# Performance work log

Hardware: AMD Instinct MI355X
Metric: run time of the kernel (lower is better)

The kernel has to match this reference:

```python
import jax, jax.numpy as jnp
import numpy as np

NUM_GRAPHS = 32

def leaky(x):
    return jax.nn.leaky_relu(x, 0.1)

def setup_inputs() -> dict:
    key = jax.random.key(0)
    ks = jax.random.split(key, 32)
    N, E = 8000, 32000
    x = jax.random.normal(ks[0], (N, 4), dtype=jnp.float32)
    edge_index = jax.random.randint(ks[1], (2, E), 0, N, dtype=jnp.int32)
    batch_index = jnp.sort(jax.random.randint(ks[2], (N,), 0, NUM_GRAPHS, dtype=jnp.int32))
    def lin(k, i, o, s=0.1):
        k1, k2 = jax.random.split(k)
        return jax.random.normal(k1, (i, o), dtype=jnp.float32) * s, jax.random.normal(k2, (o,), dtype=jnp.float32) * s
    p = {}
    # edge networks: Linear(3,64)+LeakyReLU+Linear(64, in*out)+LeakyReLU
    p['en1_w1'], p['en1_b1'] = lin(ks[3], 3, 64)
    p['en1_w2'], p['en1_b2'] = lin(ks[4], 64, 4 * 8)
    p['en2_w1'], p['en2_b1'] = lin(ks[5], 3, 64)
    p['en2_w2'], p['en2_b2'] = lin(ks[6], 64, 8 * 64)
    p['en3_w1'], p['en3_b1'] = lin(ks[7], 3, 64)
    p['en3_w2'], p['en3_b2'] = lin(ks[8], 64, 64 * 128)
    # NNConv root weights + biases
    p['root1'], p['cb1'] = lin(ks[9], 4, 8)
    p['root2'], p['cb2'] = lin(ks[10], 8, 64)
    p['root3'], p['cb3'] = lin(ks[11], 64, 128)
    # readout MLP
    p['fc1_w'], p['fc1_b'] = lin(ks[12], 128, 128)
    p['fc2_w'], p['fc2_b'] = lin(ks[13], 128, 64)
    p['fc3_w'], p['fc3_b'] = lin(ks[14], 64, 1)
    return dict(x=x, edge_index=edge_index, batch_index=batch_index, **p)

def nnconv(h, edge_index, edge_attr, w1, b1, w2, b2, root, cbias, in_ch, out_ch):
    # per-edge weight matrix from edge attributes
    e = leaky(edge_attr @ w1 + b1)              # [E,64]
    W = leaky(e @ w2 + b2).reshape(-1, in_ch, out_ch)  # [E,in,out]
    msg = jnp.einsum('ei,eio->eo', h[edge_index[0]], W)  # gather + per-edge matmul
    agg = jax.ops.segment_sum(msg, edge_index[1], num_segments=h.shape[0])  # scatter-add
    return agg + h @ root + cbias

def reference(x, edge_index, batch_index, en1_w1, en1_b1, en1_w2, en1_b2, en2_w1, en2_b1, en2_w2, en2_b2, en3_w1, en3_b1, en3_w2, en3_b2, root1, cb1, root2, cb2, root3, cb3, fc1_w, fc1_b, fc2_w, fc2_b, fc3_w, fc3_b):
    edge_attr = (x[edge_index[1]] - x[edge_index[0]])[:, 1:]  # [E,3] relative position
    h = leaky(nnconv(x, edge_index, edge_attr, en1_w1, en1_b1, en1_w2, en1_b2, root1, cb1, 4, 8))
    h = leaky(nnconv(h, edge_index, edge_attr, en2_w1, en2_b1, en2_w2, en2_b2, root2, cb2, 8, 64))
    h = leaky(nnconv(h, edge_index, edge_attr, en3_w1, en3_b1, en3_w2, en3_b2, root3, cb3, 64, 128))
    g = jax.ops.segment_sum(h, batch_index, num_segments=NUM_GRAPHS)  # sum-pool per graph
    g = leaky(g @ fc1_w + fc1_b)
    g = leaky(g @ fc2_w + fc2_b)
    return g @ fc3_w + fc3_b  # [G,1] total energies
```

## Files before the change

kernel.cpp:

```cpp
#include <hip/hip_runtime.h>
#include <hip/hip_bf16.h>

typedef __attribute__((ext_vector_type(8))) short short8;
typedef __attribute__((ext_vector_type(4))) float floatx4;
typedef __attribute__((ext_vector_type(2))) float float2v;

__device__ __forceinline__ float leaky(float v){ return v > 0.f ? v : 0.1f*v; }
__device__ __forceinline__ void atomAdd(float* p, float v){ unsafeAtomicAdd(p, v); }
__device__ __forceinline__ short f2bf(float f){
  __hip_bfloat16 h = __float2bfloat16(f);
  return *reinterpret_cast<short*>(&h);
}

__global__ void efeat_conv1(const float* __restrict__ x, const int* __restrict__ ei,
                            const float* __restrict__ w1a, const float* __restrict__ b1a,
                            const float* __restrict__ w1b, const float* __restrict__ b1b,
                            const float* __restrict__ w1c, const float* __restrict__ b1c,
                            const float* __restrict__ c1w2, const float* __restrict__ c1b2,
                            short* __restrict__ ef2b, short* __restrict__ ef3b,
                            float* __restrict__ agg1, int E, int Epad){
  __shared__ float sm[4][64];
  int tid = threadIdx.x;
  int id = blockIdx.x*256 + tid;
  int e = id >> 6, j = id & 63;
  float v1 = 0.f;
  if (e < Epad){
    if (e >= E){ ef2b[id] = 0; ef3b[id] = 0; }
    else {
      int s = ei[e], d = ei[E+e];
      float a0 = x[d*4+1] - x[s*4+1];
      float a1 = x[d*4+2] - x[s*4+2];
      float a2 = x[d*4+3] - x[s*4+3];
      v1 = leaky(a0*w1a[j] + a1*w1a[64+j] + a2*w1a[128+j] + b1a[j]);
      ef2b[id] = f2bf(leaky(a0*w1b[j] + a1*w1b[64+j] + a2*w1b[128+j] + b1b[j]));
      ef3b[id] = f2bf(leaky(a0*w1c[j] + a1*w1c[64+j] + a2*w1c[128+j] + b1c[j]));
    }
  }
  sm[tid >> 6][j] = v1;
  __syncthreads();
  if (tid < 32){
    int le = tid >> 3, o = tid & 7;
    int ge = blockIdx.x*4 + le;
    if (ge < E){
      int s = ei[ge], d = ei[E+ge];
      float z[4];
      #pragma unroll
      for (int i=0;i<4;i++) z[i] = c1b2[i*8+o];
      for (int k=0;k<64;k++){
        float a = sm[le][k];
        #pragma unroll
        for (int i=0;i<4;i++) z[i] += a*c1w2[k*32 + i*8 + o];
      }
      float msg = 0.f;
      #pragma unroll
      for (int i=0;i<4;i++) msg += x[s*4+i]*leaky(z[i]);
      atomAdd(&agg1[d*8+o], msg);
    }
  }
}

__global__ void pack_w2_all(const float* __restrict__ w2a, short* __restrict__ pa,
                            const float* __restrict__ w2b, short* __restrict__ pb){
  int bid = blockIdx.x;
  const float* w2; short* dst; int IC, OC, cbase;
  if (bid < 16){ w2 = w2a; dst = pa; IC = 8;  OC = 64;  cbase = bid*4; }
  else        { w2 = w2b; dst = pb; IC = 64; OC = 128; cbase = (bid-16)*4; }
  int lane = threadIdx.x & 63;
  int c = cbase + (threadIdx.x >> 6);
  int OT = OC/16;
  int kh = c & 1; int rem = c >> 1; int otg = rem % OT; int i = rem / OT;
  int n = lane & 15, q = lane >> 4;
  short out[8];
  #pragma unroll
  for (int j=0;j<8;j++){
    int k = kh*32 + q*8 + j;
    out[j] = f2bf(w2[(size_t)k*(IC*OC) + i*OC + otg*16 + n]);
  }
  *reinterpret_cast<short8*>(dst + (size_t)c*512 + lane*8) = *reinterpret_cast<short8*>(out);
}

template<int IC, int OC>
__global__ void node_kernel(float* __restrict__ h, const float* __restrict__ hin,
                            const float* __restrict__ root, const float* __restrict__ cb, int N){
  int id = blockIdx.x*256 + threadIdx.x;
  if (id >= N*OC) return;
  int n = id / OC, o = id % OC;
  float v = h[id] + cb[o];
  const float* hi = hin + (size_t)n*IC;
  #pragma unroll
  for (int i=0;i<IC;i++) v += hi[i]*root[i*OC+o];
  h[id] = leaky(v);
}

__global__ __launch_bounds__(256)
void node3_pool(const float* __restrict__ agg, const float* __restrict__ hin,
                const float* __restrict__ root, const float* __restrict__ cb,
                const int* __restrict__ batch, float* __restrict__ g, int N){
  __shared__ float rootS[64*128];
  __shared__ float hrow[16][64];
  int t = threadIdx.x;
  #pragma unroll
  for (int r=0;r<8;r++){
    int idx = t + r*256;
    reinterpret_cast<float4*>(rootS)[idx] = reinterpret_cast<const float4*>(root)[idx];
  }
  int n0 = blockIdx.x*16;
  {
    int nn = t >> 4, c = (t & 15)*4;
    int n = n0 + nn;
    float4 hv = (n < N) ? *reinterpret_cast<const float4*>(hin + (size_t)n*64 + c)
                        : float4{0.f,0.f,0.f,0.f};
    hrow[nn][c+0]=hv.x; hrow[nn][c+1]=hv.y; hrow[nn][c+2]=hv.z; hrow[nn][c+3]=hv.w;
  }
  __syncthreads();
  int o = t & 127, np = t >> 7;
  float acc = 0.f; int cur = -1;
  for (int rep=0; rep<8; rep++){
    int nl = rep*2 + np; int n = n0 + nl;
    if (n >= N) break;
    int b = batch[n];
    if (b != cur){ if (cur >= 0) atomAdd(&g[cur*128+o], acc); acc = 0.f; cur = b; }
    float v = agg[(size_t)n*128 + o] + cb[o];
    #pragma unroll 16
    for (int i=0;i<64;i++) v += hrow[nl][i]*rootS[i*128+o];
    acc += leaky(v);
  }
  if (cur >= 0) atomAdd(&g[cur*128+o], acc);
}

template<int IC, int OC, int MB, int ICB>
__global__ __launch_bounds__(256)
void conv_mfma(const short* __restrict__ efb, const float* __restrict__ h,
               const int* __restrict__ ei, const short* __restrict__ w2p,
               const float* __restrict__ b2, float* __restrict__ agg, int E){
  constexpr int ME   = MB*16;
  constexpr int OT   = OC/16;
  constexpr int WOT  = OT/4;
  constexpr int NSPL = IC/ICB;
  __shared__ float hsT[ICB][ME];
  __shared__ int sdst[ME];
  int tid = threadIdx.x;
  int bi = blockIdx.x;
  int eb = (bi / NSPL) * ME;
  int i0 = (bi % NSPL) * ICB;

  {
    int e = tid % ME;
    int ge = eb + e;
    bool valid = ge < E;
    int src = valid ? ei[ge] : 0;
    constexpr int CH  = 256/ME;
    constexpr int IPC = ICB/CH;
    int c = tid / ME;
    const float* hp = h + (size_t)src*IC + i0 + c*IPC;
    if constexpr (IPC == 8){
      #pragma unroll
      for (int half=0; half<2; half++){
        float4 hv = valid ? reinterpret_cast<const float4*>(hp)[half]
                          : float4{0.f,0.f,0.f,0.f};
        hsT[c*IPC + half*4 + 0][e] = hv.x;
        hsT[c*IPC + half*4 + 1][e] = hv.y;
        hsT[c*IPC + half*4 + 2][e] = hv.z;
        hsT[c*IPC + half*4 + 3][e] = hv.w;
      }
    } else {
      #pragma unroll
      for (int j=0;j<IPC;j++)
        hsT[c*IPC + j][e] = valid ? hp[j] : 0.f;
    }
    if (tid < ME) sdst[tid] = (eb + tid < E) ? ei[E + eb + tid] : -1;
  }
  __syncthreads();

  int lane = tid & 63;
  int wv = tid >> 6;
  int n = lane & 15, quad = lane >> 4;
  int o0 = wv * (OC/4);

  short8 A[MB][2];
  #pragma unroll
  for (int m=0;m<MB;m++)
    #pragma unroll
    for (int kh=0;kh<2;kh++)
      A[m][kh] = *reinterpret_cast<const short8*>(efb + (size_t)(eb + m*16 + n)*64 + kh*32 + quad*8);

  float2v msg[MB][WOT][2];
  #pragma unroll
  for (int m=0;m<MB;m++)
    #pragma unroll
    for (int t=0;t<WOT;t++){
      msg[m][t][0] = (float2v){0.f,0.f};
      msg[m][t][1] = (float2v){0.f,0.f};
    }

  auto loadB = [&](int ii, short8 (&Bt)[WOT][2], float (&bzt)[WOT]){
    int ig = i0 + ii;
    if (ig >= IC) ig = IC-1;
    #pragma unroll
    for (int t=0;t<WOT;t++){
      int otg = (o0 >> 4) + t;
      #pragma unroll
      for (int kh=0;kh<2;kh++)
        Bt[t][kh] = *reinterpret_cast<const short8*>(w2p + ((size_t)((ig*OT + otg)*2 + kh) << 9) + lane*8);
      bzt[t] = b2[ig*OC + o0 + t*16 + n];
    }
  };
  auto compute = [&](int ii, short8 (&Bt)[WOT][2], float (&bzt)[WOT]){
    #pragma unroll
    for (int m=0;m<MB;m++){
      float4 hv = *reinterpret_cast<const float4*>(&hsT[ii][m*16 + quad*4]);
      float2v hvl = {hv.x, hv.y};
      float2v hvh = {hv.z, hv.w};
      #pragma unroll
      for (int t=0;t<WOT;t++){
        floatx4 z = {bzt[t], bzt[t], bzt[t], bzt[t]};
        z = __builtin_amdgcn_mfma_f32_16x16x32_bf16(A[m][0], Bt[t][0], z, 0, 0, 0);
        z = __builtin_amdgcn_mfma_f32_16x16x32_bf16(A[m][1], Bt[t][1], z, 0, 0, 0);
        float2v zl = {z[0], z[1]};
        float2v zh = {z[2], z[3]};
        float2v ll = __builtin_elementwise_max(zl, zl*0.1f);
        float2v lh = __builtin_elementwise_max(zh, zh*0.1f);
        msg[m][t][0] += hvl*ll;
        msg[m][t][1] += hvh*lh;
      }
    }
  };

  short8 B0[WOT][2], B1[WOT][2];
  float bz0[WOT], bz1[WOT];
  loadB(0, B0, bz0);
  #pragma unroll 2
  for (int i=0;i<ICB;i+=2){
    loadB(i+1, B1, bz1);
    compute(i, B0, bz0);
    loadB(i+2, B0, bz0);
    compute(i+1, B1, bz1);
  }

  #pragma unroll
  for (int m=0;m<MB;m++){
    #pragma unroll
    for (int r=0;r<4;r++){
      int d = sdst[m*16 + quad*4 + r];
      if (d >= 0){
        #pragma unroll
        for (int t=0;t<WOT;t++)
          atomAdd(&agg[(size_t)d*OC + o0 + t*16 + n], msg[m][t][r>>1][r&1]);
      }
    }
  }
}

__global__ void head_kernel(const float* __restrict__ g,
                            const float* __restrict__ fc1w, const float* __restrict__ fc1b,
                            const float* __restrict__ fc2w, const float* __restrict__ fc2b,
                            const float* __restrict__ fc3w, const float* __restrict__ fc3b,
                            float* __restrict__ out){
  __shared__ float s1[128], s2[128];
  int gi = blockIdx.x, t = threadIdx.x;
  s1[t] = g[gi*128+t];
  __syncthreads();
  float v = fc1b[t];
  for (int i=0;i<128;i++) v += s1[i]*fc1w[i*128+t];
  s2[t] = leaky(v);
  __syncthreads();
  if (t < 64){
    float v2 = fc2b[t];
    for (int i=0;i<128;i++) v2 += s2[i]*fc2w[i*64+t];
    s1[t] = leaky(v2);
  }
  __syncthreads();
  if (t == 0){
    float v3 = fc3b[0];
    for (int i=0;i<64;i++) v3 += s1[i]*fc3w[i];
    out[gi] = v3;
  }
}

extern "C" void kernel_launch(void* const* d_in, const int* in_sizes, int n_in,
                              void* d_out, int out_size, void* d_ws, size_t ws_size,
                              hipStream_t stream) {
  const float* x      = (const float*)d_in[0];
  const int*   ei     = (const int*)  d_in[1];
  const int*   batch  = (const int*)  d_in[2];
  const float* en1_w1 = (const float*)d_in[3];  const float* en1_b1 = (const float*)d_in[4];
  const float* en1_w2 = (const float*)d_in[5];  const float* en1_b2 = (const float*)d_in[6];
  const float* en2_w1 = (const float*)d_in[7];  const float* en2_b1 = (const float*)d_in[8];
  const float* en2_w2 = (const float*)d_in[9];  const float* en2_b2 = (const float*)d_in[10];
  const float* en3_w1 = (const float*)d_in[11]; const float* en3_b1 = (const float*)d_in[12];
  const float* en3_w2 = (const float*)d_in[13]; const float* en3_b2 = (const float*)d_in[14];
  const float* root1  = (const float*)d_in[15]; const float* cb1    = (const float*)d_in[16];
  const float* root2  = (const float*)d_in[17]; const float* cb2    = (const float*)d_in[18];
  const float* root3  = (const float*)d_in[19]; const float* cb3    = (const float*)d_in[20];
  const float* fc1w   = (const float*)d_in[21]; const float* fc1b   = (const float*)d_in[22];
  const float* fc2w   = (const float*)d_in[23]; const float* fc2b   = (const float*)d_in[24];
  const float* fc3w   = (const float*)d_in[25]; const float* fc3b   = (const float*)d_in[26];
  float* out = (float*)d_out;

  const int N = in_sizes[0] / 4;
  const int E = in_sizes[1] / 2;
  const int G = 32;
  const int Epad = (E + 63) & ~63;

  short* ef2b = (short*)d_ws;
  short* ef3b = ef2b + (size_t)Epad*64;
  short* w2p2 = ef3b + (size_t)Epad*64;
  short* w2p3 = w2p2 + 8*4*2*512;
  float* a1   = (float*)(w2p3 + 64*8*2*512);
  float* a2   = a1 + (size_t)N*8;
  float* a3   = a2 + (size_t)N*64;
  float* g    = a3 + (size_t)N*128;

  size_t zero_bytes = ((size_t)N*(8+64+128) + (size_t)G*128) * sizeof(float);
  hipMemsetAsync(a1, 0, zero_bytes, stream);

  efeat_conv1<<<Epad/4, 256, 0, stream>>>(
      x, ei, en1_w1, en1_b1, en2_w1, en2_b1, en3_w1, en3_b1,
      en1_w2, en1_b2, ef2b, ef3b, a1, E, Epad);

  pack_w2_all<<<272, 256, 0, stream>>>(en2_w2, w2p2, en3_w2, w2p3);

  node_kernel<4,8><<<(N*8 + 255)/256, 256, 0, stream>>>(a1, x, root1, cb1, N);

  conv_mfma<8,64,2,8><<<Epad/32, 256, 0, stream>>>(ef2b, a1, ei, w2p2, en2_b2, a2, E);
  node_kernel<8,64><<<(N*64 + 255)/256, 256, 0, stream>>>(a2, a1, root2, cb2, N);

  conv_mfma<64,128,4,32><<<(Epad/64)*2, 256, 0, stream>>>(ef3b, a2, ei, w2p3, en3_b2, a3, E);
  node3_pool<<<(N + 15)/16, 256, 0, stream>>>(a3, a2, root3, cb3, batch, g, N);

  head_kernel<<<G, 128, 0, stream>>>(g, fc1w, fc1b, fc2w, fc2b, fc3w, fc3b, out);
}
```

Measured before the change: 251.2 us.

## Fuse all GNN stages into one cooperative persistent kernel with grid syncs

Replaces the memset plus eight separate kernel launches with a single cooperative persistent kernel. Stages are separated by grid.sync(), shared memory is reused across stages through a union, and edge-network first-layer weights are staged in LDS. This removes launch and inter-kernel gaps. In exchange it limits the grid to resident blocks and adds grid-wide barrier costs. Register pressure from the merged kernel may lower occupancy for the MFMA conv stages.

```diff
diff --git a/kernel.cpp b/kernel.cpp
--- a/kernel.cpp
+++ b/kernel.cpp
@@ -1,5 +1,8 @@
 #include <hip/hip_runtime.h>
 #include <hip/hip_bf16.h>
+#include <hip/hip_cooperative_groups.h>
+
+namespace cg = cooperative_groups;
 
 typedef __attribute__((ext_vector_type(8))) short short8;
 typedef __attribute__((ext_vector_type(4))) float floatx4;
@@ -12,145 +15,43 @@
   return *reinterpret_cast<short*>(&h);
 }
 
-__global__ void efeat_conv1(const float* __restrict__ x, const int* __restrict__ ei,
-                            const float* __restrict__ w1a, const float* __restrict__ b1a,
-                            const float* __restrict__ w1b, const float* __restrict__ b1b,
-                            const float* __restrict__ w1c, const float* __restrict__ b1c,
-                            const float* __restrict__ c1w2, const float* __restrict__ c1b2,
-                            short* __restrict__ ef2b, short* __restrict__ ef3b,
-                            float* __restrict__ agg1, int E, int Epad){
-  __shared__ float sm[4][64];
+struct MegaP {
+  const float *x; const int *ei; const int *batch;
+  const float *en1_w1,*en1_b1,*en1_w2,*en1_b2;
+  const float *en2_w1,*en2_b1,*en2_w2,*en2_b2;
+  const float *en3_w1,*en3_b1,*en3_w2,*en3_b2;
+  const float *root1,*cb1,*root2,*cb2,*root3,*cb3;
+  const float *fc1w,*fc1b,*fc2w,*fc2b,*fc3w,*fc3b;
+  short *ef2b,*ef3b,*w2p2,*w2p3;
+  float *a1,*a2,*a3,*g,*out;
+  int N,E,Epad;
+};
+
+struct SMem {
+  union {
+    struct { float hsT[32*64]; int sdst[64]; } c3;
+    struct { float hsT[8*32];  int sdst[32]; } c2;
+    struct { float rootS[8192]; float hrow[16][64]; } np;
+    struct { float w1s[3][192]; float b1s[3][64]; float c1w2s[2048];
+             float c1b2s[32]; float sm[4][64]; } ef;
+    struct { float s1[128]; float s2[128]; } hd;
+  };
+};
+
+template<int IC, int OC, int MB, int ICB>
+__device__ __forceinline__ void conv_unit(float* hsT, int* sdst,
+    const short* __restrict__ efb, const float* __restrict__ h,
+    const int* __restrict__ ei, const short* __restrict__ w2p,
+    const float* __restrict__ b2, float* __restrict__ agg,
+    int E, int eb, int i0){
+  constexpr int ME = MB*16, OT = OC/16, WOT = OT/4;
   int tid = threadIdx.x;
-  int id = blockIdx.x*256 + tid;
-  int e = id >> 6, j = id & 63;
-  float v1 = 0.f;
-  if (e < Epad){
-    if (e >= E){ ef2b[id] = 0; ef3b[id] = 0; }
-    else {
-      int s = ei[e], d = ei[E+e];
-      float a0 = x[d*4+1] - x[s*4+1];
-      float a1 = x[d*4+2] - x[s*4+2];
-      float a2 = x[d*4+3] - x[s*4+3];
-      v1 = leaky(a0*w1a[j] + a1*w1a[64+j] + a2*w1a[128+j] + b1a[j]);
-      ef2b[id] = f2bf(leaky(a0*w1b[j] + a1*w1b[64+j] + a2*w1b[128+j] + b1b[j]));
-      ef3b[id] = f2bf(leaky(a0*w1c[j] + a1*w1c[64+j] + a2*w1c[128+j] + b1c[j]));
-    }
-  }
-  sm[tid >> 6][j] = v1;
-  __syncthreads();
-  if (tid < 32){
-    int le = tid >> 3, o = tid & 7;
-    int ge = blockIdx.x*4 + le;
-    if (ge < E){
-      int s = ei[ge], d = ei[E+ge];
-      float z[4];
-      #pragma unroll
-      for (int i=0;i<4;i++) z[i] = c1b2[i*8+o];
-      for (int k=0;k<64;k++){
-        float a = sm[le][k];
-        #pragma unroll
-        for (int i=0;i<4;i++) z[i] += a*c1w2[k*32 + i*8 + o];
-      }
-      float msg = 0.f;
-      #pragma unroll
-      for (int i=0;i<4;i++) msg += x[s*4+i]*leaky(z[i]);
-      atomAdd(&agg1[d*8+o], msg);
-    }
-  }
-}
-
-__global__ void pack_w2_all(const float* __restrict__ w2a, short* __restrict__ pa,
-                            const float* __restrict__ w2b, short* __restrict__ pb){
-  int bid = blockIdx.x;
-  const float* w2; short* dst; int IC, OC, cbase;
-  if (bid < 16){ w2 = w2a; dst = pa; IC = 8;  OC = 64;  cbase = bid*4; }
-  else        { w2 = w2b; dst = pb; IC = 64; OC = 128; cbase = (bid-16)*4; }
-  int lane = threadIdx.x & 63;
-  int c = cbase + (threadIdx.x >> 6);
-  int OT = OC/16;
-  int kh = c & 1; int rem = c >> 1; int otg = rem % OT; int i = rem / OT;
-  int n = lane & 15, q = lane >> 4;
-  short out[8];
-  #pragma unroll
-  for (int j=0;j<8;j++){
-    int k = kh*32 + q*8 + j;
-    out[j] = f2bf(w2[(size_t)k*(IC*OC) + i*OC + otg*16 + n]);
-  }
-  *reinterpret_cast<short8*>(dst + (size_t)c*512 + lane*8) = *reinterpret_cast<short8*>(out);
-}
-
-template<int IC, int OC>
-__global__ void node_kernel(float* __restrict__ h, const float* __restrict__ hin,
-                            const float* __restrict__ root, const float* __restrict__ cb, int N){
-  int id = blockIdx.x*256 + threadIdx.x;
-  if (id >= N*OC) return;
-  int n = id / OC, o = id % OC;
-  float v = h[id] + cb[o];
-  const float* hi = hin + (size_t)n*IC;
-  #pragma unroll
-  for (int i=0;i<IC;i++) v += hi[i]*root[i*OC+o];
-  h[id] = leaky(v);
-}
-
-__global__ __launch_bounds__(256)
-void node3_pool(const float* __restrict__ agg, const float* __restrict__ hin,
-                const float* __restrict__ root, const float* __restrict__ cb,
-                const int* __restrict__ batch, float* __restrict__ g, int N){
-  __shared__ float rootS[64*128];
-  __shared__ float hrow[16][64];
-  int t = threadIdx.x;
-  #pragma unroll
-  for (int r=0;r<8;r++){
-    int idx = t + r*256;
-    reinterpret_cast<float4*>(rootS)[idx] = reinterpret_cast<const float4*>(root)[idx];
-  }
-  int n0 = blockIdx.x*16;
-  {
-    int nn = t >> 4, c = (t & 15)*4;
-    int n = n0 + nn;
-    float4 hv = (n < N) ? *reinterpret_cast<const float4*>(hin + (size_t)n*64 + c)
-                        : float4{0.f,0.f,0.f,0.f};
-    hrow[nn][c+0]=hv.x; hrow[nn][c+1]=hv.y; hrow[nn][c+2]=hv.z; hrow[nn][c+3]=hv.w;
-  }
-  __syncthreads();
-  int o = t & 127, np = t >> 7;
-  float acc = 0.f; int cur = -1;
-  for (int rep=0; rep<8; rep++){
-    int nl = rep*2 + np; int n = n0 + nl;
-    if (n >= N) break;
-    int b = batch[n];
-    if (b != cur){ if (cur >= 0) atomAdd(&g[cur*128+o], acc); acc = 0.f; cur = b; }
-    float v = agg[(size_t)n*128 + o] + cb[o];
-    #pragma unroll 16
-    for (int i=0;i<64;i++) v += hrow[nl][i]*rootS[i*128+o];
-    acc += leaky(v);
-  }
-  if (cur >= 0) atomAdd(&g[cur*128+o], acc);
-}
-
-template<int IC, int OC, int MB, int ICB>
-__global__ __launch_bounds__(256)
-void conv_mfma(const short* __restrict__ efb, const float* __restrict__ h,
-               const int* __restrict__ ei, const short* __restrict__ w2p,
-               const float* __restrict__ b2, float* __restrict__ agg, int E){
-  constexpr int ME   = MB*16;
-  constexpr int OT   = OC/16;
-  constexpr int WOT  = OT/4;
-  constexpr int NSPL = IC/ICB;
-  __shared__ float hsT[ICB][ME];
-  __shared__ int sdst[ME];
-  int tid = threadIdx.x;
-  int bi = blockIdx.x;
-  int eb = (bi / NSPL) * ME;
-  int i0 = (bi % NSPL) * ICB;
-
   {
     int e = tid % ME;
     int ge = eb + e;
     bool valid = ge < E;
     int src = valid ? ei[ge] : 0;
-    constexpr int CH  = 256/ME;
-    constexpr int IPC = ICB/CH;
+    constexpr int CH = 256/ME, IPC = ICB/CH;
     int c = tid / ME;
     const float* hp = h + (size_t)src*IC + i0 + c*IPC;
     if constexpr (IPC == 8){
@@ -158,22 +59,21 @@
       for (int half=0; half<2; half++){
         float4 hv = valid ? reinterpret_cast<const float4*>(hp)[half]
                           : float4{0.f,0.f,0.f,0.f};
-        hsT[c*IPC + half*4 + 0][e] = hv.x;
-        hsT[c*IPC + half*4 + 1][e] = hv.y;
-        hsT[c*IPC + half*4 + 2][e] = hv.z;
-        hsT[c*IPC + half*4 + 3][e] = hv.w;
+        hsT[(c*IPC+half*4+0)*ME + e] = hv.x;
+        hsT[(c*IPC+half*4+1)*ME + e] = hv.y;
+        hsT[(c*IPC+half*4+2)*ME + e] = hv.z;
+        hsT[(c*IPC+half*4+3)*ME + e] = hv.w;
       }
     } else {
       #pragma unroll
       for (int j=0;j<IPC;j++)
-        hsT[c*IPC + j][e] = valid ? hp[j] : 0.f;
+        hsT[(c*IPC+j)*ME + e] = valid ? hp[j] : 0.f;
     }
     if (tid < ME) sdst[tid] = (eb + tid < E) ? ei[E + eb + tid] : -1;
   }
   __syncthreads();
 
-  int lane = tid & 63;
-  int wv = tid >> 6;
+  int lane = tid & 63, wv = tid >> 6;
   int n = lane & 15, quad = lane >> 4;
   int o0 = wv * (OC/4);
 
@@ -194,8 +94,8 @@
     }
 
   auto loadB = [&](int ii, short8 (&Bt)[WOT][2], float (&bzt)[WOT]){
-    int ig = i0 + ii;
-    if (ig >= IC) ig = IC-1;
+    int il = (ii < ICB) ? ii : (ICB-1);
+    int ig = i0 + il;
     #pragma unroll
     for (int t=0;t<WOT;t++){
       int otg = (o0 >> 4) + t;
@@ -208,7 +108,7 @@
   auto compute = [&](int ii, short8 (&Bt)[WOT][2], float (&bzt)[WOT]){
     #pragma unroll
     for (int m=0;m<MB;m++){
-      float4 hv = *reinterpret_cast<const float4*>(&hsT[ii][m*16 + quad*4]);
+      float4 hv = *reinterpret_cast<const float4*>(&hsT[ii*ME + m*16 + quad*4]);
       float2v hvl = {hv.x, hv.y};
       float2v hvh = {hv.z, hv.w};
       #pragma unroll
@@ -249,84 +149,225 @@
       }
     }
   }
+  __syncthreads();
 }
 
-__global__ void head_kernel(const float* __restrict__ g,
-                            const float* __restrict__ fc1w, const float* __restrict__ fc1b,
-                            const float* __restrict__ fc2w, const float* __restrict__ fc2b,
-                            const float* __restrict__ fc3w, const float* __restrict__ fc3b,
-                            float* __restrict__ out){
-  __shared__ float s1[128], s2[128];
-  int gi = blockIdx.x, t = threadIdx.x;
-  s1[t] = g[gi*128+t];
-  __syncthreads();
-  float v = fc1b[t];
-  for (int i=0;i<128;i++) v += s1[i]*fc1w[i*128+t];
-  s2[t] = leaky(v);
-  __syncthreads();
-  if (t < 64){
-    float v2 = fc2b[t];
-    for (int i=0;i<128;i++) v2 += s2[i]*fc2w[i*64+t];
-    s1[t] = leaky(v2);
-  }
-  __syncthreads();
-  if (t == 0){
-    float v3 = fc3b[0];
-    for (int i=0;i<64;i++) v3 += s1[i]*fc3w[i];
-    out[gi] = v3;
+__global__ __launch_bounds__(256, 4) void mega(MegaP p){
+  cg::grid_group grid = cg::this_grid();
+  __shared__ SMem S;
+  const int tid = threadIdx.x, bid = blockIdx.x, nb = gridDim.x;
+  const int N = p.N, E = p.E, Epad = p.Epad;
+
+  {
+    size_t zn = (size_t)N*(8+64+128) + 32*128;
+    for (size_t i = (size_t)bid*256 + tid; i < zn; i += (size_t)nb*256) p.a1[i] = 0.f;
+    for (int t = bid*256 + tid; t < 1088*64; t += nb*256){
+      int lane = t & 63, c = t >> 6;
+      const float* w2; short* dst; int ICOC, OT, cc;
+      if (c < 64){ w2 = p.en2_w2; dst = p.w2p2; ICOC = 512;  OT = 4; cc = c; }
+      else       { w2 = p.en3_w2; dst = p.w2p3; ICOC = 8192; OT = 8; cc = c - 64; }
+      int kh = cc & 1, rem = cc >> 1, otg = rem % OT, i = rem / OT;
+      int n = lane & 15, q = lane >> 4;
+      short o8[8];
+      #pragma unroll
+      for (int j=0;j<8;j++){
+        int k = kh*32 + q*8 + j;
+        o8[j] = f2bf(w2[(size_t)k*ICOC + i*(OT*16) + otg*16 + n]);
+      }
+      *reinterpret_cast<short8*>(dst + (size_t)cc*512 + lane*8) = *reinterpret_cast<short8*>(o8);
+    }
+  }
+  grid.sync();
+
+  {
+    for (int idx = tid; idx < 576; idx += 256){
+      int net = idx / 192, r = idx % 192;
+      S.ef.w1s[net][r] = (net==0 ? p.en1_w1 : net==1 ? p.en2_w1 : p.en3_w1)[r];
+    }
+    if (tid < 192){
+      int net = tid >> 6, j = tid & 63;
+      S.ef.b1s[net][j] = (net==0 ? p.en1_b1 : net==1 ? p.en2_b1 : p.en3_b1)[j];
+    }
+    for (int idx = tid; idx < 2048; idx += 256) S.ef.c1w2s[idx] = p.en1_w2[idx];
+    if (tid < 32) S.ef.c1b2s[tid] = p.en1_b2[tid];
+    __syncthreads();
+    int nunits = Epad/4;
+    for (int u = bid; u < nunits; u += nb){
+      int e = u*4 + (tid >> 6), j = tid & 63;
+      float v1 = 0.f;
+      if (e >= E){
+        p.ef2b[(size_t)e*64 + j] = 0; p.ef3b[(size_t)e*64 + j] = 0;
+      } else {
+        int s = p.ei[e], d = p.ei[E+e];
+        float4 xs = *reinterpret_cast<const float4*>(p.x + (size_t)s*4);
+        float4 xd = *reinterpret_cast<const float4*>(p.x + (size_t)d*4);
+        float d0 = xd.y - xs.y, d1 = xd.z - xs.z, d2 = xd.w - xs.w;
+        v1 = leaky(d0*S.ef.w1s[0][j] + d1*S.ef.w1s[0][64+j] + d2*S.ef.w1s[0][128+j] + S.ef.b1s[0][j]);
+        p.ef2b[(size_t)e*64+j] = f2bf(leaky(d0*S.ef.w1s[1][j] + d1*S.ef.w1s[1][64+j] + d2*S.ef.w1s[1][128+j] + S.ef.b1s[1][j]));
+        p.ef3b[(size_t)e*64+j] = f2bf(leaky(d0*S.ef.w1s[2][j] + d1*S.ef.w1s[2][64+j] + d2*S.ef.w1s[2][128+j] + S.ef.b1s[2][j]));
+      }
+      S.ef.sm[tid >> 6][j] = v1;
+      __syncthreads();
+      if (tid < 32){
+        int le = tid >> 3, o = tid & 7;
+        int ge = u*4 + le;
+        if (ge < E){
+          int s = p.ei[ge], d = p.ei[E+ge];
+          float z[4];
+          #pragma unroll
+          for (int i=0;i<4;i++) z[i] = S.ef.c1b2s[i*8+o];
+          for (int k=0;k<64;k++){
+            float a = S.ef.sm[le][k];
+            #pragma unroll
+            for (int i=0;i<4;i++) z[i] += a*S.ef.c1w2s[k*32 + i*8 + o];
+          }
+          float4 xv = *reinterpret_cast<const float4*>(p.x + (size_t)s*4);
+          float msg = xv.x*leaky(z[0]) + xv.y*leaky(z[1]) + xv.z*leaky(z[2]) + xv.w*leaky(z[3]);
+          atomAdd(&p.a1[(size_t)d*8 + o], msg);
+        }
+      }
+      __syncthreads();
+    }
+  }
+  grid.sync();
+
+  for (int id = bid*256 + tid; id < N*8; id += nb*256){
+    int nn = id >> 3, o = id & 7;
+    float v = p.a1[id] + p.cb1[o];
+    float4 xv = *reinterpret_cast<const float4*>(p.x + (size_t)nn*4);
+    v += xv.x*p.root1[o] + xv.y*p.root1[8+o] + xv.z*p.root1[16+o] + xv.w*p.root1[24+o];
+    p.a1[id] = leaky(v);
+  }
+  grid.sync();
+
+  {
+    int nunits = Epad/32;
+    for (int u = bid; u < nunits; u += nb)
+      conv_unit<8,64,2,8>(S.c2.hsT, S.c2.sdst, p.ef2b, p.a1, p.ei, p.w2p2, p.en2_b2, p.a2, E, u*32, 0);
+  }
+  grid.sync();
+
+  for (int id = bid*256 + tid; id < N*16; id += nb*256){
+    int nn = id >> 4, o0 = (id & 15)*4;
+    const float* hi = p.a1 + (size_t)nn*8;
+    float4 v  = *reinterpret_cast<float4*>(p.a2 + (size_t)nn*64 + o0);
+    float4 cbv = *reinterpret_cast<const float4*>(p.cb2 + o0);
+    v.x += cbv.x; v.y += cbv.y; v.z += cbv.z; v.w += cbv.w;
+    #pragma unroll
+    for (int i=0;i<8;i++){
+      float hv = hi[i];
+      float4 rv = *reinterpret_cast<const float4*>(p.root2 + i*64 + o0);
+      v.x += hv*rv.x; v.y += hv*rv.y; v.z += hv*rv.z; v.w += hv*rv.w;
+    }
+    v.x = leaky(v.x); v.y = leaky(v.y); v.z = leaky(v.z); v.w = leaky(v.w);
+    *reinterpret_cast<float4*>(p.a2 + (size_t)nn*64 + o0) = v;
+  }
+  grid.sync();
+
+  {
+    int nunits = (Epad/64)*2;
+    for (int u = bid; u < nunits; u += nb)
+      conv_unit<64,128,4,32>(S.c3.hsT, S.c3.sdst, p.ef3b, p.a2, p.ei, p.w2p3, p.en3_b2, p.a3, E, (u>>1)*64, (u&1)*32);
+  }
+  grid.sync();
+
+  {
+    for (int r = tid; r < 2048; r += 256)
+      reinterpret_cast<float4*>(S.np.rootS)[r] = reinterpret_cast<const float4*>(p.root3)[r];
+    __syncthreads();
+    int nunits = (N + 15)/16;
+    for (int u = bid; u < nunits; u += nb){
+      int n0 = u*16;
+      {
+        int nn = tid >> 4, c = (tid & 15)*4;
+        int n = n0 + nn;
+        float4 hv = (n < N) ? *reinterpret_cast<const float4*>(p.a2 + (size_t)n*64 + c)
+                            : float4{0.f,0.f,0.f,0.f};
+        S.np.hrow[nn][c+0]=hv.x; S.np.hrow[nn][c+1]=hv.y; S.np.hrow[nn][c+2]=hv.z; S.np.hrow[nn][c+3]=hv.w;
+      }
+      __syncthreads();
+      int o = tid & 127, np_ = tid >> 7;
+      float acc = 0.f; int cur = -1;
+      for (int rep=0; rep<8; rep++){
+        int nl = rep*2 + np_; int n = n0 + nl;
+        if (n >= N) break;
+        int b = p.batch[n];
+        if (b != cur){ if (cur >= 0) atomAdd(&p.g[cur*128+o], acc); acc = 0.f; cur = b; }
+        float v = p.a3[(size_t)n*128 + o] + p.cb3[o];
+        #pragma unroll 16
+        for (int i=0;i<64;i++) v += S.np.hrow[nl][i]*S.np.rootS[i*128+o];
+        acc += leaky(v);
+      }
+      if (cur >= 0) atomAdd(&p.g[cur*128+o], acc);
+      __syncthreads();
+    }
+  }
+  grid.sync();
+
+  if (bid < 32){
+    int t = tid;
+    if (t < 128) S.hd.s1[t] = p.g[bid*128 + t];
+    __syncthreads();
+    if (t < 128){
+      float v = p.fc1b[t];
+      for (int i=0;i<128;i++) v += S.hd.s1[i]*p.fc1w[i*128+t];
+      S.hd.s2[t] = leaky(v);
+    }
+    __syncthreads();
+    if (t < 64){
+      float v2 = p.fc2b[t];
+      for (int i=0;i<128;i++) v2 += S.hd.s2[i]*p.fc2w[i*64+t];
+      S.hd.s1[t] = leaky(v2);
+    }
+    __syncthreads();
+    if (t == 0){
+      float v3 = p.fc3b[0];
+      for (int i=0;i<64;i++) v3 += S.hd.s1[i]*p.fc3w[i];
+      p.out[bid] = v3;
+    }
   }
 }
 
 extern "C" void kernel_launch(void* const* d_in, const int* in_sizes, int n_in,
                               void* d_out, int out_size, void* d_ws, size_t ws_size,
                               hipStream_t stream) {
-  const float* x      = (const float*)d_in[0];
-  const int*   ei     = (const int*)  d_in[1];
-  const int*   batch  = (const int*)  d_in[2];
-  const float* en1_w1 = (const float*)d_in[3];  const float* en1_b1 = (const float*)d_in[4];
-  const float* en1_w2 = (const float*)d_in[5];  const float* en1_b2 = (const float*)d_in[6];
-  const float* en2_w1 = (const float*)d_in[7];  const float* en2_b1 = (const float*)d_in[8];
-  const float* en2_w2 = (const float*)d_in[9];  const float* en2_b2 = (const float*)d_in[10];
-  const float* en3_w1 = (const float*)d_in[11]; const float* en3_b1 = (const float*)d_in[12];
-  const float* en3_w2 = (const float*)d_in[13]; const float* en3_b2 = (const float*)d_in[14];
-  const float* root1  = (const float*)d_in[15]; const float* cb1    = (const float*)d_in[16];
-  const float* root2  = (const float*)d_in[17]; const float* cb2    = (const float*)d_in[18];
-  const float* root3  = (const float*)d_in[19]; const float* cb3    = (const float*)d_in[20];
-  const float* fc1w   = (const float*)d_in[21]; const float* fc1b   = (const float*)d_in[22];
-  const float* fc2w   = (const float*)d_in[23]; const float* fc2b   = (const float*)d_in[24];
-  const float* fc3w   = (const float*)d_in[25]; const float* fc3b   = (const float*)d_in[26];
-  float* out = (float*)d_out;
-
-  const int N = in_sizes[0] / 4;
-  const int E = in_sizes[1] / 2;
-  const int G = 32;
-  const int Epad = (E + 63) & ~63;
-
-  short* ef2b = (short*)d_ws;
-  short* ef3b = ef2b + (size_t)Epad*64;
-  short* w2p2 = ef3b + (size_t)Epad*64;
-  short* w2p3 = w2p2 + 8*4*2*512;
-  float* a1   = (float*)(w2p3 + 64*8*2*512);
-  float* a2   = a1 + (size_t)N*8;
-  float* a3   = a2 + (size_t)N*64;
-  float* g    = a3 + (size_t)N*128;
-
-  size_t zero_bytes = ((size_t)N*(8+64+128) + (size_t)G*128) * sizeof(float);
-  hipMemsetAsync(a1, 0, zero_bytes, stream);
-
-  efeat_conv1<<<Epad/4, 256, 0, stream>>>(
-      x, ei, en1_w1, en1_b1, en2_w1, en2_b1, en3_w1, en3_b1,
-      en1_w2, en1_b2, ef2b, ef3b, a1, E, Epad);
-
-  pack_w2_all<<<272, 256, 0, stream>>>(en2_w2, w2p2, en3_w2, w2p3);
-
-  node_kernel<4,8><<<(N*8 + 255)/256, 256, 0, stream>>>(a1, x, root1, cb1, N);
-
-  conv_mfma<8,64,2,8><<<Epad/32, 256, 0, stream>>>(ef2b, a1, ei, w2p2, en2_b2, a2, E);
-  node_kernel<8,64><<<(N*64 + 255)/256, 256, 0, stream>>>(a2, a1, root2, cb2, N);
-
-  conv_mfma<64,128,4,32><<<(Epad/64)*2, 256, 0, stream>>>(ef3b, a2, ei, w2p3, en3_b2, a3, E);
-  node3_pool<<<(N + 15)/16, 256, 0, stream>>>(a3, a2, root3, cb3, batch, g, N);
-
-  head_kernel<<<G, 128, 0, stream>>>(g, fc1w, fc1b, fc2w, fc2b, fc3w, fc3b, out);
+  MegaP prm;
+  prm.x      = (const float*)d_in[0];
+  prm.ei     = (const int*)  d_in[1];
+  prm.batch  = (const int*)  d_in[2];
+  prm.en1_w1 = (const float*)d_in[3];  prm.en1_b1 = (const float*)d_in[4];
+  prm.en1_w2 = (const float*)d_in[5];  prm.en1_b2 = (const float*)d_in[6];
+  prm.en2_w1 = (const float*)d_in[7];  prm.en2_b1 = (const float*)d_in[8];
+  prm.en2_w2 = (const float*)d_in[9];  prm.en2_b2 = (const float*)d_in[10];
+  prm.en3_w1 = (const float*)d_in[11]; prm.en3_b1 = (const float*)d_in[12];
+  prm.en3_w2 = (const float*)d_in[13]; prm.en3_b2 = (const float*)d_in[14];
+  prm.root1  = (const float*)d_in[15]; prm.cb1    = (const float*)d_in[16];
+  prm.root2  = (const float*)d_in[17]; prm.cb2    = (const float*)d_in[18];
+  prm.root3  = (const float*)d_in[19]; prm.cb3    = (const float*)d_in[20];
+  prm.fc1w   = (const float*)d_in[21]; prm.fc1b   = (const float*)d_in[22];
+  prm.fc2w   = (const float*)d_in[23]; prm.fc2b   = (const float*)d_in[24];
+  prm.fc3w   = (const float*)d_in[25]; prm.fc3b   = (const float*)d_in[26];
+  prm.out = (float*)d_out;
+
+  prm.N = in_sizes[0] / 4;
+  prm.E = in_sizes[1] / 2;
+  prm.Epad = (prm.E + 63) & ~63;
+
+  prm.ef2b = (short*)d_ws;
+  prm.ef3b = prm.ef2b + (size_t)prm.Epad*64;
+  prm.w2p2 = prm.ef3b + (size_t)prm.Epad*64;
+  prm.w2p3 = prm.w2p2 + 8*4*2*512;
+  prm.a1   = (float*)(prm.w2p3 + 64*8*2*512);
+  prm.a2   = prm.a1 + (size_t)prm.N*8;
+  prm.a3   = prm.a2 + (size_t)prm.N*64;
+  prm.g    = prm.a3 + (size_t)prm.N*128;
+
+  int maxB = 0;
+  hipOccupancyMaxActiveBlocksPerMultiprocessor(&maxB, mega, 256, 0);
+  int grid = maxB * 256;
+  if (grid > 1024) grid = 1024;
+  if (grid < 256)  grid = 256;
+
+  void* args[] = { &prm };
+  hipLaunchCooperativeKernel((const void*)mega, dim3(grid), dim3(256), args, 0, stream);
 }
```

Measured after the change: 731.7 us. +191.3%, slower.
